# Kernel optimization log

Measured on AMD Instinct MI355X. Metric: run time of the kernel, lower is better.

The kernel has to match this reference:

```python
import jax, jax.numpy as jnp
import numpy as np

N = 100000       # nodes
E = 1600000      # edges
F_IN = 128       # input features
HID = 64         # hidden dim
CLS = 16         # classes


def setup_inputs() -> dict:
    key = jax.random.key(0)
    k = jax.random.split(key, 6)
    x = jax.random.normal(k[0], (N, F_IN), dtype=jnp.float32)
    src = jax.random.randint(k[1], (E,), 0, N, dtype=jnp.int32)
    dst = jax.random.randint(k[2], (E,), 0, N, dtype=jnp.int32)
    edge_index = jnp.stack([src, dst], axis=0)
    W1 = jax.random.normal(k[3], (F_IN, HID), dtype=jnp.float32) * (1.0 / np.sqrt(F_IN))
    b1 = jnp.zeros((HID,), dtype=jnp.float32)
    W2 = jax.random.normal(k[4], (HID, CLS), dtype=jnp.float32) * (1.0 / np.sqrt(HID))
    b2 = jnp.zeros((CLS,), dtype=jnp.float32)
    return {"x": x, "edge_index": edge_index, "W1": W1, "b1": b1, "W2": W2, "b2": b2}


def gcn_conv(x, W, b, src, dst, n_nodes):
    # GCNConv(normalize=True): h = W x; out_i = sum_{j->i} h_j / sqrt(d_i d_j) + h_i / d_i + b
    # (self-loops added with weight 1; deg includes the self-loop)
    h = x @ W                                             # [N, out]
    ones = jnp.ones(src.shape[0], dtype=x.dtype)
    deg = jax.ops.segment_sum(ones, dst, num_segments=n_nodes) + 1.0   # [N]
    dinv = deg ** -0.5
    norm = dinv[src] * dinv[dst]                          # [E]
    msg = h[src] * norm[:, None]                          # [E, out] gather
    out = jax.ops.segment_sum(msg, dst, num_segments=n_nodes)          # scatter-add
    out = out + h * (1.0 / deg)[:, None] + b              # self-loop term + bias
    return out


def reference(x, edge_index, W1, b1, W2, b2):
    src, dst = edge_index[0], edge_index[1]
    n = x.shape[0]
    h = jax.nn.relu(gcn_conv(x, W1, b1, src, dst, n))
    # dropout(p=0.5) is identity in eval mode
    h = jax.nn.relu(gcn_conv(h, W2, b2, src, dst, n))
    return jax.nn.log_softmax(h, axis=-1)
```

## Files before the change

### kernel.cpp

```cpp
#include <hip/hip_runtime.h>
#include <hip/hip_bf16.h>


typedef unsigned short u16;
typedef __attribute__((ext_vector_type(8))) short short8;
typedef __attribute__((ext_vector_type(4))) float f32x4;

#define CAP 4096

__device__ __forceinline__ float bf2f(u16 u) {
  return __uint_as_float(((unsigned int)u) << 16);
}
__device__ __forceinline__ u16 f2bf(float f) {
  unsigned int u = __float_as_uint(f);
  u += 0x7fffu + ((u >> 16) & 1u);
  return (u16)(u >> 16);
}
__device__ __forceinline__ float blo(unsigned int u) {
  return __uint_as_float(u << 16);
}
__device__ __forceinline__ float bhi(unsigned int u) {
  return __uint_as_float(u & 0xffff0000u);
}

__global__ __launch_bounds__(512) void kpartc(
    const int* __restrict__ src, const int* __restrict__ dst,
    int* __restrict__ cursor, int* __restrict__ etmp,
    const void* __restrict__ W1r, const void* __restrict__ b1r,
    const void* __restrict__ W2r, const void* __restrict__ b2r,
    u16* __restrict__ W1t, float* __restrict__ b1f, u16* __restrict__ W2b,
    float* __restrict__ b2f, int* __restrict__ mode, int E, int NB) {
  __shared__ int hist[1024], basep[1024];
  __shared__ float red[8];
  __shared__ int smode;
  int tid = threadIdx.x;

  if (blockIdx.x == 0) {
    const u16* w = (const u16*)W1r;
    float mx = 0.f;
    for (int i = tid; i < 8192; i += 512) {
      float av = fabsf(bf2f(w[i]));
      if (!(av <= 1e6f)) av = 3e38f;
      mx = fmaxf(mx, av);
    }
    #pragma unroll
    for (int off = 32; off >= 1; off >>= 1) mx = fmaxf(mx, __shfl_xor(mx, off, 64));
    if ((tid & 63) == 0) red[tid >> 6] = mx;
    __syncthreads();
    if (tid == 0) {
      float m2 = 0.f;
      #pragma unroll
      for (int wv = 0; wv < 8; ++wv) m2 = fmaxf(m2, red[wv]);
      smode = (m2 > 1e6f) ? 1 : 0;
      mode[0] = smode;
    }
    __syncthreads();
    int m = smode;
    for (int i = tid; i < 8192; i += 512) {
      int f = i >> 9, l = (i >> 3) & 63, j = i & 7;
      int k = (f >> 2) * 32 + (l >> 4) * 8 + j;
      int n = (f & 3) * 16 + (l & 15);
      int s = k * 64 + n;
      W1t[i] = m ? f2bf(((const float*)W1r)[s]) : ((const u16*)W1r)[s];
    }
    for (int i = tid; i < 1024; i += 512)
      W2b[i] = m ? f2bf(((const float*)W2r)[i]) : ((const u16*)W2r)[i];
    if (tid < 64) b1f[tid] = m ? ((const float*)b1r)[tid] : bf2f(((const u16*)b1r)[tid]);
    if (tid < 16) b2f[tid] = m ? ((const float*)b2r)[tid] : bf2f(((const u16*)b2r)[tid]);
    return;
  }

  for (int i = tid; i < 1024; i += 512) hist[i] = 0;
  __syncthreads();
  int e0 = (blockIdx.x - 1) * 4096 + tid * 8;
  int pk[8], off[8], cb[8];
  if (e0 + 7 < E) {
    int4 s4[2], d4[2];
    #pragma unroll
    for (int u = 0; u < 2; ++u) {
      s4[u] = ((const int4*)(src + e0))[u];
      d4[u] = ((const int4*)(dst + e0))[u];
    }
    const int* sp = (const int*)s4;
    const int* dp = (const int*)d4;
    #pragma unroll
    for (int k = 0; k < 8; ++k) {
      int s = sp[k], d = dp[k];
      cb[k] = d >> 7;
      pk[k] = (s << 7) | (d & 127);
      off[k] = atomicAdd(&hist[cb[k]], 1);
    }
  } else {
    #pragma unroll
    for (int k = 0; k < 8; ++k) {
      int e = e0 + k;
      cb[k] = -1;
      if (e < E) {
        int s = src[e], d = dst[e];
        cb[k] = d >> 7;
        pk[k] = (s << 7) | (d & 127);
        off[k] = atomicAdd(&hist[cb[k]], 1);
      }
    }
  }
  __syncthreads();
  for (int i = tid; i < NB; i += 512)
    if (hist[i]) basep[i] = atomicAdd(&cursor[i], hist[i]);
  __syncthreads();
  if (e0 + 7 < E) {
    #pragma unroll
    for (int k = 0; k < 8; ++k)
      etmp[cb[k] * CAP + basep[cb[k]] + off[k]] = pk[k];
  } else {
    #pragma unroll
    for (int k = 0; k < 8; ++k)
      if (cb[k] >= 0) etmp[cb[k] * CAP + basep[cb[k]] + off[k]] = pk[k];
  }
}

__global__ __launch_bounds__(256) void ksort(
    const int* __restrict__ etmp, const int* __restrict__ cursor,
    float* __restrict__ dinv, int* __restrict__ esort,
    int2* __restrict__ rowse, u16* __restrict__ h1s, u16* __restrict__ h2sb,
    int N) {
  __shared__ int hist[128], starts[128], curs[128];
  int tid = threadIdx.x;
  int bk = blockIdx.x;
  int base = bk * CAP;
  int cnt = cursor[bk];
  int node0 = bk << 7;

  if (bk == 0) {
    if (tid < 8) ((uint4*)h1s)[(size_t)N * 8 + tid] = make_uint4(0, 0, 0, 0);
    if (tid < 2) ((uint4*)h2sb)[(size_t)N * 2 + tid] = make_uint4(0, 0, 0, 0);
  }

  if (tid < 128) hist[tid] = 0;
  __syncthreads();
  for (int i = tid; i < cnt; i += 256)
    atomicAdd(&hist[etmp[base + i] & 127], 1);
  __syncthreads();
  if (tid < 64) {
    int v0 = hist[tid], v1 = hist[tid + 64];
    int p0 = (v0 + 7) & ~7, p1 = (v1 + 7) & ~7;
    int s0 = p0;
    #pragma unroll
    for (int off = 1; off < 64; off <<= 1) {
      int t = __shfl_up(s0, off, 64);
      if (tid >= off) s0 += t;
    }
    int tot0 = __shfl(s0, 63, 64);
    int s1 = p1;
    #pragma unroll
    for (int off = 1; off < 64; off <<= 1) {
      int t = __shfl_up(s1, off, 64);
      if (tid >= off) s1 += t;
    }
    s1 += tot0;
    int st0 = s0 - p0, st1 = s1 - p1;
    starts[tid] = st0;       starts[tid + 64] = st1;
    curs[tid] = st0;         curs[tid + 64] = st1;
    int n0 = node0 + tid, n1 = n0 + 64;
    if (n0 < N) {
      rowse[n0] = make_int2(base + st0, base + st0 + p0);
      dinv[n0] = rsqrtf((float)(v0 + 1));
    }
    if (n1 < N) {
      rowse[n1] = make_int2(base + st1, base + st1 + p1);
      dinv[n1] = rsqrtf((float)(v1 + 1));
    }
  }
  __syncthreads();
  if (tid < 128) {
    int v = hist[tid], st = starts[tid];
    int p = (v + 7) & ~7;
    for (int j = v; j < p; ++j) esort[base + st + j] = N;
  }
  for (int i = tid; i < cnt; i += 256) {
    int pk = etmp[base + i];
    int pos = atomicAdd(&curs[pk & 127], 1);
    esort[base + pos] = pk >> 7;
  }
}

__global__ __launch_bounds__(256, 6) void kgemm1(
    const void* __restrict__ xraw, const u16* __restrict__ W1t,
    const int* __restrict__ mode, const float* __restrict__ dinv,
    u16* __restrict__ h1s, int N) {
  int tid = threadIdx.x;
  int mflag = mode[0];
  int lane = tid & 63, wv = tid >> 6;
  int m16 = lane & 15, q = lane >> 4;
  int row0 = blockIdx.x * 64 + wv * 16;

  f32x4 acc[4];
  #pragma unroll
  for (int jb = 0; jb < 4; ++jb) acc[jb] = (f32x4){0.f, 0.f, 0.f, 0.f};

  int rowm = row0 + m16;
  size_t rc = (size_t)((rowm < N) ? rowm : (N - 1));
  #pragma unroll
  for (int kb = 0; kb < 4; ++kb) {
    short8 a;
    if (mflag) {
      const float* xf = (const float*)xraw + rc * 128 + kb * 32 + q * 8;
      float4 u0 = ((const float4*)xf)[0];
      float4 u1 = ((const float4*)xf)[1];
      __hip_bfloat162 p0 = __float22bfloat162_rn(make_float2(u0.x, u0.y));
      __hip_bfloat162 p1 = __float22bfloat162_rn(make_float2(u0.z, u0.w));
      __hip_bfloat162 p2 = __float22bfloat162_rn(make_float2(u1.x, u1.y));
      __hip_bfloat162 p3 = __float22bfloat162_rn(make_float2(u1.z, u1.w));
      unsigned int w0 = *(const unsigned int*)&p0;
      unsigned int w1 = *(const unsigned int*)&p1;
      unsigned int w2 = *(const unsigned int*)&p2;
      unsigned int w3 = *(const unsigned int*)&p3;
      a[0] = (short)(w0 & 0xffff); a[1] = (short)(w0 >> 16);
      a[2] = (short)(w1 & 0xffff); a[3] = (short)(w1 >> 16);
      a[4] = (short)(w2 & 0xffff); a[5] = (short)(w2 >> 16);
      a[6] = (short)(w3 & 0xffff); a[7] = (short)(w3 >> 16);
    } else {
      a = *(const short8*)((const u16*)xraw + rc * 128 + kb * 32 + q * 8);
    }
    #pragma unroll
    for (int jb = 0; jb < 4; ++jb) {
      short8 bwf = *(const short8*)(W1t + (size_t)((kb * 4 + jb) * 64 + lane) * 8);
      acc[jb] = __builtin_amdgcn_mfma_f32_16x16x32_bf16(a, bwf, acc[jb], 0, 0, 0);
    }
  }

  int r4 = row0 + q * 4;
  float4 dvv = (r4 + 3 < N) ? *(const float4*)(dinv + r4)
                            : make_float4(0.f, 0.f, 0.f, 0.f);
  float dv[4] = {dvv.x, dvv.y, dvv.z, dvv.w};
  if (r4 + 3 >= N) {
    #pragma unroll
    for (int r = 0; r < 4; ++r) dv[r] = (r4 + r < N) ? dinv[r4 + r] : 0.f;
  }
  #pragma unroll
  for (int r = 0; r < 4; ++r) {
    int rr = r4 + r;
    if (rr < N) {
      #pragma unroll
      for (int jb = 0; jb < 4; ++jb)
        h1s[(size_t)rr * 64 + jb * 16 + m16] = f2bf(acc[jb][r] * dv[r]);
    }
  }
}

__global__ __launch_bounds__(256) void kagg1f(
    const u16* __restrict__ h1s, const int* __restrict__ esort,
    const int2* __restrict__ rowse, const float* __restrict__ dinv,
    const float* __restrict__ b1f, const u16* __restrict__ W2b,
    u16* __restrict__ h2sb, int N) {
  __shared__ __align__(16) u16 sA[4][16 * 72];
  __shared__ float sdv[4][16];
  int tid = threadIdx.x;
  int lane = tid & 63, wv = tid >> 6;
  int o = lane >> 3, fl = lane & 7;
  int wbase = blockIdx.x * 64 + wv * 16;

  const uint4* __restrict__ h1v4 = (const uint4*)h1s;

  #pragma unroll
  for (int sub = 0; sub < 2; ++sub) {
    int nloc = sub * 8 + o;
    int node = wbase + nloc;
    int cn = (node < N) ? node : (N - 1);
    int2 se = (node < N) ? rowse[node] : make_int2(0, 0);
    int beg = se.x, end = se.y;
    float a0 = 0.f, a1 = 0.f, a2 = 0.f, a3 = 0.f;
    float a4 = 0.f, a5 = 0.f, a6 = 0.f, a7 = 0.f;

    int k = beg;
    int myi = (k < end) ? esort[k + fl] : 0;
    while (k < end) {
      int cur = myi;
      int kn = k + 8;
      if (kn < end) myi = esort[kn + fl];
      uint4 g[8];
      #pragma unroll
      for (int p = 0; p < 8; ++p) {
        int s = __shfl(cur, (o << 3) + p, 64);
        g[p] = h1v4[s * 8 + fl];
      }
      #pragma unroll
      for (int p = 0; p < 8; ++p) {
        a0 += blo(g[p].x); a1 += bhi(g[p].x);
        a2 += blo(g[p].y); a3 += bhi(g[p].y);
        a4 += blo(g[p].z); a5 += bhi(g[p].z);
        a6 += blo(g[p].w); a7 += bhi(g[p].w);
      }
      k = kn;
    }

    uint4 sg = h1v4[cn * 8 + fl];
    float dv = dinv[cn];
    float4 bva = ((const float4*)b1f)[fl * 2];
    float4 bvb = ((const float4*)b1f)[fl * 2 + 1];
    float v0 = fmaxf(dv * (a0 + blo(sg.x)) + bva.x, 0.f);
    float v1 = fmaxf(dv * (a1 + bhi(sg.x)) + bva.y, 0.f);
    float v2 = fmaxf(dv * (a2 + blo(sg.y)) + bva.z, 0.f);
    float v3 = fmaxf(dv * (a3 + bhi(sg.y)) + bva.w, 0.f);
    float v4 = fmaxf(dv * (a4 + blo(sg.z)) + bvb.x, 0.f);
    float v5 = fmaxf(dv * (a5 + bhi(sg.z)) + bvb.y, 0.f);
    float v6 = fmaxf(dv * (a6 + blo(sg.w)) + bvb.z, 0.f);
    float v7 = fmaxf(dv * (a7 + bhi(sg.w)) + bvb.w, 0.f);
    uint4 st;
    st.x = (unsigned int)f2bf(v0) | ((unsigned int)f2bf(v1) << 16);
    st.y = (unsigned int)f2bf(v2) | ((unsigned int)f2bf(v3) << 16);
    st.z = (unsigned int)f2bf(v4) | ((unsigned int)f2bf(v5) << 16);
    st.w = (unsigned int)f2bf(v6) | ((unsigned int)f2bf(v7) << 16);
    *(uint4*)&sA[wv][nloc * 72 + fl * 8] = st;
    if (fl == 0) sdv[wv][nloc] = dv;
  }

  int m16 = lane & 15, q = lane >> 4;
  short8 bw0, bw1;
  #pragma unroll
  for (int j = 0; j < 8; ++j) {
    bw0[j] = (short)W2b[(q * 8 + j) * 16 + m16];
    bw1[j] = (short)W2b[(32 + q * 8 + j) * 16 + m16];
  }
  __builtin_amdgcn_wave_barrier();

  const u16* ar = &sA[wv][m16 * 72];
  short8 af0 = *(const short8*)(ar + q * 8);
  short8 af1 = *(const short8*)(ar + 32 + q * 8);
  f32x4 c = (f32x4){0.f, 0.f, 0.f, 0.f};
  c = __builtin_amdgcn_mfma_f32_16x16x32_bf16(af0, bw0, c, 0, 0, 0);
  c = __builtin_amdgcn_mfma_f32_16x16x32_bf16(af1, bw1, c, 0, 0, 0);
  #pragma unroll
  for (int r = 0; r < 4; ++r) {
    int nloc2 = q * 4 + r;
    int nd2 = wbase + nloc2;
    if (nd2 < N) h2sb[(size_t)nd2 * 16 + m16] = f2bf(c[r] * sdv[wv][nloc2]);
  }
}

__global__ __launch_bounds__(256) void kagg2(
    const u16* __restrict__ h2sb, const int* __restrict__ esort,
    const int2* __restrict__ rowse, const float* __restrict__ dinv,
    const float* __restrict__ b2f, const int* __restrict__ mode,
    void* __restrict__ out, int n) {
  int mflag = mode[0];
  int tid = threadIdx.x;
  int lane = tid & 63, wv = tid >> 6;
  int oc = lane >> 3, ol = lane & 7;
  int hl = ol >> 2, fl = ol & 3;
  int node = blockIdx.x * 32 + wv * 8 + oc;
  if (node >= n) node = n - 1;
  int2 se = rowse[node];
  int beg = se.x, end = se.y;
  const uint2* h2v = (const uint2*)h2sb;
  uint2 sg = h2v[node * 4 + fl];
  float a0 = 0.f, a1 = 0.f, a2 = 0.f, a3 = 0.f;

  for (int k = beg; k < end; k += 8) {
    int i0 = esort[k + hl], i1 = esort[k + 2 + hl];
    int i2 = esort[k + 4 + hl], i3 = esort[k + 6 + hl];
    uint2 g0 = h2v[i0 * 4 + fl];
    uint2 g1 = h2v[i1 * 4 + fl];
    uint2 g2 = h2v[i2 * 4 + fl];
    uint2 g3 = h2v[i3 * 4 + fl];
    a0 += bf2f((u16)(g0.x & 0xffff)) + bf2f((u16)(g1.x & 0xffff))
        + bf2f((u16)(g2.x & 0xffff)) + bf2f((u16)(g3.x & 0xffff));
    a1 += bf2f((u16)(g0.x >> 16)) + bf2f((u16)(g1.x >> 16))
        + bf2f((u16)(g2.x >> 16)) + bf2f((u16)(g3.x >> 16));
    a2 += bf2f((u16)(g0.y & 0xffff)) + bf2f((u16)(g1.y & 0xffff))
        + bf2f((u16)(g2.y & 0xffff)) + bf2f((u16)(g3.y & 0xffff));
    a3 += bf2f((u16)(g0.y >> 16)) + bf2f((u16)(g1.y >> 16))
        + bf2f((u16)(g2.y >> 16)) + bf2f((u16)(g3.y >> 16));
  }
  a0 += __shfl_xor(a0, 4, 8);  a1 += __shfl_xor(a1, 4, 8);
  a2 += __shfl_xor(a2, 4, 8);  a3 += __shfl_xor(a3, 4, 8);

  float dv = dinv[node];
  float4 bv = ((const float4*)b2f)[fl];
  float v0 = fmaxf(dv * (a0 + bf2f((u16)(sg.x & 0xffff))) + bv.x, 0.f);
  float v1 = fmaxf(dv * (a1 + bf2f((u16)(sg.x >> 16))) + bv.y, 0.f);
  float v2 = fmaxf(dv * (a2 + bf2f((u16)(sg.y & 0xffff))) + bv.z, 0.f);
  float v3 = fmaxf(dv * (a3 + bf2f((u16)(sg.y >> 16))) + bv.w, 0.f);

  float m = fmaxf(fmaxf(v0, v1), fmaxf(v2, v3));
  m = fmaxf(m, __shfl_xor(m, 1, 4));
  m = fmaxf(m, __shfl_xor(m, 2, 4));
  float ex = __expf(v0 - m) + __expf(v1 - m) + __expf(v2 - m) + __expf(v3 - m);
  ex += __shfl_xor(ex, 1, 4);
  ex += __shfl_xor(ex, 2, 4);
  float lg = __logf(ex);
  float r0 = v0 - m - lg, r1 = v1 - m - lg;
  float r2 = v2 - m - lg, r3 = v3 - m - lg;
  if (hl == 0) {
    if (mflag) {
      ((float4*)out)[(size_t)node * 4 + fl] = make_float4(r0, r1, r2, r3);
    } else {
      uint2 o;
      o.x = (unsigned int)f2bf(r0) | ((unsigned int)f2bf(r1) << 16);
      o.y = (unsigned int)f2bf(r2) | ((unsigned int)f2bf(r3) << 16);
      ((uint2*)out)[(size_t)node * 4 + fl] = o;
    }
  }
}

extern "C" void kernel_launch(void* const* d_in, const int* in_sizes, int n_in,
                              void* d_out, int out_size, void* d_ws, size_t ws_size,
                              hipStream_t stream) {
  const void* x  = d_in[0];
  const int* ei  = (const int*)d_in[1];
  const void* W1 = d_in[2];
  const void* b1 = d_in[3];
  const void* W2 = d_in[4];
  const void* b2 = d_in[5];

  const int N = in_sizes[0] / 128;
  const int E = in_sizes[1] / 2;
  const int* src = ei;
  const int* dst = ei + E;
  const int NB = (N + 127) >> 7;

  char* ws = (char*)d_ws;
  size_t off = 0;
  auto alloc = [&](size_t bytes) -> char* {
    char* p = ws + off;
    off = (off + bytes + 255) & ~(size_t)255;
    return p;
  };
  u16*   h1s    = (u16*)  alloc((size_t)(N + 1) * 64 * 2);
  u16*   h2sb   = (u16*)  alloc((size_t)(N + 1) * 16 * 2);
  int*   etmp   = (int*)  alloc((size_t)NB * CAP * 4);
  int*   esort  = (int*)  alloc((size_t)NB * CAP * 4);
  int2*  rowse  = (int2*) alloc((size_t)N * 8);
  float* dinv   = (float*)alloc((size_t)N * 4);
  int*   cursor = (int*)  alloc((size_t)NB * 4);
  u16*   W1t    = (u16*)  alloc(8192 * 2);
  u16*   W2b    = (u16*)  alloc(1024 * 2);
  float* b1f    = (float*)alloc(64 * 4);
  float* b2f    = (float*)alloc(16 * 4);
  int*   mode   = (int*)  alloc(4);

  hipMemsetAsync(cursor, 0, (size_t)NB * 4, stream);

  int pblocks = (E + 4095) / 4096;
  kpartc<<<pblocks + 1, 512, 0, stream>>>(src, dst, cursor, etmp,
                                          W1, b1, W2, b2,
                                          W1t, b1f, W2b, b2f, mode, E, NB);
  ksort<<<NB, 256, 0, stream>>>(etmp, cursor, dinv, esort, rowse,
                                h1s, h2sb, N);
  kgemm1<<<(N + 63) / 64, 256, 0, stream>>>(x, W1t, mode, dinv, h1s, N);
  kagg1f<<<(N + 63) / 64, 256, 0, stream>>>(h1s, esort, rowse, dinv, b1f, W2b,
                                            h2sb, N);
  kagg2<<<(N + 31) / 32, 256, 0, stream>>>(h2sb, esort, rowse, dinv, b2f, mode,
                                           d_out, N);
}
```

Baseline: 188.6 us.

## Coarsen edge buckets to 512 destination nodes and widen sort blocks

The counting-sort preprocessing now groups edges into buckets of 512 destination nodes instead of 128. That cuts the bucket count about fourfold, reducing global cursor atomics and spreading each partition block's scattered writes over fewer, denser regions. The partition kernel now handles 4 edges per thread (2048 per block), and the per-bucket sort kernel uses 512 threads with a two-level wave scan. The trade-off is fewer sort blocks, around 196, which may underfill the GPU, plus a fixed per-bucket capacity of 12288 that must hold padded rows.

```diff
diff --git a/kernel.cpp b/kernel.cpp
--- a/kernel.cpp
+++ b/kernel.cpp
@@ -6,7 +6,7 @@
 typedef __attribute__((ext_vector_type(8))) short short8;
 typedef __attribute__((ext_vector_type(4))) float f32x4;
 
-#define CAP 4096
+#define CAP2 12288
 
 __device__ __forceinline__ float bf2f(u16 u) {
   return __uint_as_float(((unsigned int)u) << 16);
@@ -29,8 +29,8 @@
     const void* __restrict__ W1r, const void* __restrict__ b1r,
     const void* __restrict__ W2r, const void* __restrict__ b2r,
     u16* __restrict__ W1t, float* __restrict__ b1f, u16* __restrict__ W2b,
-    float* __restrict__ b2f, int* __restrict__ mode, int E, int NB) {
-  __shared__ int hist[1024], basep[1024];
+    float* __restrict__ b2f, int* __restrict__ mode, int E, int NB2) {
+  __shared__ int hist[256], basep[256];
   __shared__ float red[8];
   __shared__ int smode;
   int tid = threadIdx.x;
@@ -70,116 +70,103 @@
     return;
   }
 
-  for (int i = tid; i < 1024; i += 512) hist[i] = 0;
-  __syncthreads();
-  int e0 = (blockIdx.x - 1) * 4096 + tid * 8;
-  int pk[8], off[8], cb[8];
-  if (e0 + 7 < E) {
-    int4 s4[2], d4[2];
-    #pragma unroll
-    for (int u = 0; u < 2; ++u) {
-      s4[u] = ((const int4*)(src + e0))[u];
-      d4[u] = ((const int4*)(dst + e0))[u];
-    }
-    const int* sp = (const int*)s4;
-    const int* dp = (const int*)d4;
-    #pragma unroll
-    for (int k = 0; k < 8; ++k) {
+  for (int i = tid; i < 256; i += 512) hist[i] = 0;
+  if (tid < 256 && tid >= 0) {}
+  if (tid < 256) hist[tid] = 0;
+  __syncthreads();
+  int e0 = (blockIdx.x - 1) * 2048 + tid * 4;
+  int pk[4], off[4], cb[4];
+  if (e0 + 3 < E) {
+    int4 s4 = *(const int4*)(src + e0);
+    int4 d4 = *(const int4*)(dst + e0);
+    const int sp[4] = {s4.x, s4.y, s4.z, s4.w};
+    const int dp[4] = {d4.x, d4.y, d4.z, d4.w};
+    #pragma unroll
+    for (int k = 0; k < 4; ++k) {
       int s = sp[k], d = dp[k];
-      cb[k] = d >> 7;
-      pk[k] = (s << 7) | (d & 127);
+      cb[k] = d >> 9;
+      pk[k] = (s << 9) | (d & 511);
       off[k] = atomicAdd(&hist[cb[k]], 1);
     }
   } else {
     #pragma unroll
-    for (int k = 0; k < 8; ++k) {
+    for (int k = 0; k < 4; ++k) {
       int e = e0 + k;
       cb[k] = -1;
       if (e < E) {
         int s = src[e], d = dst[e];
-        cb[k] = d >> 7;
-        pk[k] = (s << 7) | (d & 127);
+        cb[k] = d >> 9;
+        pk[k] = (s << 9) | (d & 511);
         off[k] = atomicAdd(&hist[cb[k]], 1);
       }
     }
   }
   __syncthreads();
-  for (int i = tid; i < NB; i += 512)
-    if (hist[i]) basep[i] = atomicAdd(&cursor[i], hist[i]);
-  __syncthreads();
-  if (e0 + 7 < E) {
-    #pragma unroll
-    for (int k = 0; k < 8; ++k)
-      etmp[cb[k] * CAP + basep[cb[k]] + off[k]] = pk[k];
+  if (tid < NB2)
+    if (hist[tid]) basep[tid] = atomicAdd(&cursor[tid], hist[tid]);
+  __syncthreads();
+  if (e0 + 3 < E) {
+    #pragma unroll
+    for (int k = 0; k < 4; ++k)
+      etmp[cb[k] * CAP2 + basep[cb[k]] + off[k]] = pk[k];
   } else {
     #pragma unroll
-    for (int k = 0; k < 8; ++k)
-      if (cb[k] >= 0) etmp[cb[k] * CAP + basep[cb[k]] + off[k]] = pk[k];
-  }
-}
-
-__global__ __launch_bounds__(256) void ksort(
+    for (int k = 0; k < 4; ++k)
+      if (cb[k] >= 0) etmp[cb[k] * CAP2 + basep[cb[k]] + off[k]] = pk[k];
+  }
+}
+
+__global__ __launch_bounds__(512) void ksort(
     const int* __restrict__ etmp, const int* __restrict__ cursor,
     float* __restrict__ dinv, int* __restrict__ esort,
     int2* __restrict__ rowse, u16* __restrict__ h1s, u16* __restrict__ h2sb,
     int N) {
-  __shared__ int hist[128], starts[128], curs[128];
+  __shared__ int hist[512], curs[512];
+  __shared__ int wtot[8];
   int tid = threadIdx.x;
   int bk = blockIdx.x;
-  int base = bk * CAP;
+  int base = bk * CAP2;
   int cnt = cursor[bk];
-  int node0 = bk << 7;
+  int node0 = bk << 9;
 
   if (bk == 0) {
     if (tid < 8) ((uint4*)h1s)[(size_t)N * 8 + tid] = make_uint4(0, 0, 0, 0);
     if (tid < 2) ((uint4*)h2sb)[(size_t)N * 2 + tid] = make_uint4(0, 0, 0, 0);
   }
 
-  if (tid < 128) hist[tid] = 0;
-  __syncthreads();
-  for (int i = tid; i < cnt; i += 256)
-    atomicAdd(&hist[etmp[base + i] & 127], 1);
-  __syncthreads();
-  if (tid < 64) {
-    int v0 = hist[tid], v1 = hist[tid + 64];
-    int p0 = (v0 + 7) & ~7, p1 = (v1 + 7) & ~7;
-    int s0 = p0;
-    #pragma unroll
-    for (int off = 1; off < 64; off <<= 1) {
-      int t = __shfl_up(s0, off, 64);
-      if (tid >= off) s0 += t;
-    }
-    int tot0 = __shfl(s0, 63, 64);
-    int s1 = p1;
-    #pragma unroll
-    for (int off = 1; off < 64; off <<= 1) {
-      int t = __shfl_up(s1, off, 64);
-      if (tid >= off) s1 += t;
-    }
-    s1 += tot0;
-    int st0 = s0 - p0, st1 = s1 - p1;
-    starts[tid] = st0;       starts[tid + 64] = st1;
-    curs[tid] = st0;         curs[tid + 64] = st1;
-    int n0 = node0 + tid, n1 = n0 + 64;
-    if (n0 < N) {
-      rowse[n0] = make_int2(base + st0, base + st0 + p0);
-      dinv[n0] = rsqrtf((float)(v0 + 1));
-    }
-    if (n1 < N) {
-      rowse[n1] = make_int2(base + st1, base + st1 + p1);
-      dinv[n1] = rsqrtf((float)(v1 + 1));
-    }
-  }
-  __syncthreads();
-  if (tid < 128) {
-    int v = hist[tid], st = starts[tid];
-    int p = (v + 7) & ~7;
-    for (int j = v; j < p; ++j) esort[base + st + j] = N;
-  }
-  for (int i = tid; i < cnt; i += 256) {
+  hist[tid] = 0;
+  __syncthreads();
+  for (int i = tid; i < cnt; i += 512)
+    atomicAdd(&hist[etmp[base + i] & 511], 1);
+  __syncthreads();
+
+  int lane = tid & 63, wv = tid >> 6;
+  int v = hist[tid];
+  int p = (v + 7) & ~7;
+  int s = p;
+  #pragma unroll
+  for (int off = 1; off < 64; off <<= 1) {
+    int t = __shfl_up(s, off, 64);
+    if (lane >= off) s += t;
+  }
+  if (lane == 63) wtot[wv] = s;
+  __syncthreads();
+  int pre = 0;
+  #pragma unroll
+  for (int w = 0; w < 8; ++w) pre += (w < wv) ? wtot[w] : 0;
+  int st = pre + s - p;
+  curs[tid] = st;
+  int nd = node0 + tid;
+  if (nd < N) {
+    rowse[nd] = make_int2(base + st, base + st + p);
+    dinv[nd] = rsqrtf((float)(v + 1));
+  }
+  __syncthreads();
+  for (int j = v; j < p; ++j) esort[base + st + j] = N;
+  for (int i = tid; i < cnt; i += 512) {
     int pk = etmp[base + i];
-    int pos = atomicAdd(&curs[pk & 127], 1);
-    esort[base + pos] = pk >> 7;
+    int pos = atomicAdd(&curs[pk & 511], 1);
+    esort[base + pos] = pk >> 9;
   }
 }
 
@@ -416,7 +403,7 @@
   const int E = in_sizes[1] / 2;
   const int* src = ei;
   const int* dst = ei + E;
-  const int NB = (N + 127) >> 7;
+  const int NB2 = (N + 511) >> 9;
 
   char* ws = (char*)d_ws;
   size_t off = 0;
@@ -427,25 +414,25 @@
   };
   u16*   h1s    = (u16*)  alloc((size_t)(N + 1) * 64 * 2);
   u16*   h2sb   = (u16*)  alloc((size_t)(N + 1) * 16 * 2);
-  int*   etmp   = (int*)  alloc((size_t)NB * CAP * 4);
-  int*   esort  = (int*)  alloc((size_t)NB * CAP * 4);
+  int*   etmp   = (int*)  alloc((size_t)NB2 * CAP2 * 4);
+  int*   esort  = (int*)  alloc((size_t)NB2 * CAP2 * 4);
   int2*  rowse  = (int2*) alloc((size_t)N * 8);
   float* dinv   = (float*)alloc((size_t)N * 4);
-  int*   cursor = (int*)  alloc((size_t)NB * 4);
+  int*   cursor = (int*)  alloc((size_t)NB2 * 4);
   u16*   W1t    = (u16*)  alloc(8192 * 2);
   u16*   W2b    = (u16*)  alloc(1024 * 2);
   float* b1f    = (float*)alloc(64 * 4);
   float* b2f    = (float*)alloc(16 * 4);
   int*   mode   = (int*)  alloc(4);
 
-  hipMemsetAsync(cursor, 0, (size_t)NB * 4, stream);
-
-  int pblocks = (E + 4095) / 4096;
+  hipMemsetAsync(cursor, 0, (size_t)NB2 * 4, stream);
+
+  int pblocks = (E + 2047) / 2048;
   kpartc<<<pblocks + 1, 512, 0, stream>>>(src, dst, cursor, etmp,
                                           W1, b1, W2, b2,
-                                          W1t, b1f, W2b, b2f, mode, E, NB);
-  ksort<<<NB, 256, 0, stream>>>(etmp, cursor, dinv, esort, rowse,
-                                h1s, h2sb, N);
+                                          W1t, b1f, W2b, b2f, mode, E, NB2);
+  ksort<<<NB2, 512, 0, stream>>>(etmp, cursor, dinv, esort, rowse,
+                                 h1s, h2sb, N);
   kgemm1<<<(N + 63) / 64, 256, 0, stream>>>(x, W1t, mode, dinv, h1s, N);
   kagg1f<<<(N + 63) / 64, 256, 0, stream>>>(h1s, esort, rowse, dinv, b1f, W2b,
                                             h2sb, N);
```

Measured after the change: 191.6 us. No clear change (+1.6%).
